# Kernel tuning notes

Measured on AMD Instinct MI355X. Metric: run time of the kernel, lower is better.

## Reference

```python
import jax, jax.numpy as jnp
import numpy as np

LSTM_SIZE = 32
NUM_OPS = 64
NUM_EDGE = 128
TEMPERATURE = 5.0
TANH_CONST = 2.5


def _lstm_cell(x, h, c, W_ih, W_hh, b_ih, b_hh):
    # PyTorch gate order: i, f, g, o
    g = x @ W_ih.T + b_ih + h @ W_hh.T + b_hh  # [4*H]
    i, f, gg, o = jnp.split(g, 4)
    c2 = jax.nn.sigmoid(f) * c + jax.nn.sigmoid(i) * jnp.tanh(gg)
    h2 = jax.nn.sigmoid(o) * jnp.tanh(c2)
    return h2, c2


def setup_inputs() -> dict:
    key = jax.random.key(0)
    ks = jax.random.split(key, 12)
    H, G, O = LSTM_SIZE, 4 * LSTM_SIZE, NUM_OPS
    s = 0.1
    return {
        "input_vars": jax.random.uniform(ks[0], (1, 1, H), jnp.float32, -s, s),
        "W_ih0": jax.random.uniform(ks[1], (G, H), jnp.float32, -s, s),
        "W_hh0": jax.random.uniform(ks[2], (G, H), jnp.float32, -s, s),
        "b_ih0": jax.random.uniform(ks[3], (G,), jnp.float32, -s, s),
        "b_hh0": jax.random.uniform(ks[4], (G,), jnp.float32, -s, s),
        "W_ih1": jax.random.uniform(ks[5], (G, H), jnp.float32, -s, s),
        "W_hh1": jax.random.uniform(ks[6], (G, H), jnp.float32, -s, s),
        "b_ih1": jax.random.uniform(ks[7], (G,), jnp.float32, -s, s),
        "b_hh1": jax.random.uniform(ks[8], (G,), jnp.float32, -s, s),
        "embd": jax.random.uniform(ks[9], (O, H), jnp.float32, -s, s),
        "W_pred": jax.random.uniform(ks[10], (O, H), jnp.float32, -s, s),
        "b_pred": jax.random.uniform(ks[11], (O,), jnp.float32, -s, s),
        "num_edge": NUM_EDGE,
    }


def reference(input_vars, W_ih0, W_hh0, b_ih0, b_hh0,
              W_ih1, W_hh1, b_ih1, b_hh1,
              embd, W_pred, b_pred, num_edge):
    H = input_vars.shape[-1]
    x0 = input_vars.reshape(H)
    z = jnp.zeros((H,), input_vars.dtype)
    key0 = jax.random.key(42)

    def step(carry, _):
        key, x, h0, c0, h1, c1 = carry
        h0, c0 = _lstm_cell(x, h0, c0, W_ih0, W_hh0, b_ih0, b_hh0)
        h1, c1 = _lstm_cell(h0, h1, c1, W_ih1, W_hh1, b_ih1, b_hh1)
        logits = TANH_CONST * jnp.tanh((h1 @ W_pred.T + b_pred) / TEMPERATURE)
        key, sub = jax.random.split(key)
        idx = jax.random.categorical(sub, logits)
        logp = jax.nn.log_softmax(logits)
        lp = logp[idx]
        ent = -jnp.sum(jnp.exp(logp) * logp)
        x = embd[idx]
        return (key, x, h0, c0, h1, c1), (lp, ent, idx)

    _, (lps, ents, arch) = jax.lax.scan(step, (key0, x0, z, z, z, z), None, length=num_edge)
    return jnp.sum(lps), jnp.sum(ents), arch
```

## Files before the change

kernel.cpp:

```cpp
#include <hip/hip_runtime.h>
#include <stdint.h>

namespace {

typedef float v2f __attribute__((ext_vector_type(2)));
typedef int   v2i __attribute__((ext_vector_type(2)));

constexpr int H      = 32;
constexpr int NEDGE  = 128;
constexpr float TINY   = 1.1754943508222875e-38f;
constexpr float L2E    = 1.4426950408889634f;
constexpr float LN2    = 0.6931471805599453f;

__device__ __forceinline__ void tf_round(uint32_t& x0, uint32_t& x1, int r) {
  x0 += x1;
  x1 = (x1 << r) | (x1 >> (32 - r));
  x1 ^= x0;
}

__device__ __forceinline__ void tf2x32(uint32_t k0, uint32_t k1,
                                       uint32_t& x0, uint32_t& x1) {
  const uint32_t ks2 = k0 ^ k1 ^ 0x1BD11BDAu;
  x0 += k0; x1 += k1;
  tf_round(x0,x1,13); tf_round(x0,x1,15); tf_round(x0,x1,26); tf_round(x0,x1, 6);
  x0 += k1;  x1 += ks2 + 1u;
  tf_round(x0,x1,17); tf_round(x0,x1,29); tf_round(x0,x1,16); tf_round(x0,x1,24);
  x0 += ks2; x1 += k0 + 2u;
  tf_round(x0,x1,13); tf_round(x0,x1,15); tf_round(x0,x1,26); tf_round(x0,x1, 6);
  x0 += k0;  x1 += k1 + 3u;
  tf_round(x0,x1,17); tf_round(x0,x1,29); tf_round(x0,x1,16); tf_round(x0,x1,24);
  x0 += k1;  x1 += ks2 + 4u;
  tf_round(x0,x1,13); tf_round(x0,x1,15); tf_round(x0,x1,26); tf_round(x0,x1, 6);
  x0 += ks2; x1 += k0 + 5u;
}

__device__ __forceinline__ float fexp(float x) {
  return __builtin_amdgcn_exp2f(x * L2E);
}
__device__ __forceinline__ float flog(float x) {
  return __builtin_amdgcn_logf(x) * LN2;
}
__device__ __forceinline__ float fsigmoid(float x) {
  return __builtin_amdgcn_rcpf(1.0f + __builtin_amdgcn_exp2f(-x * L2E));
}
__device__ __forceinline__ float ftanh(float x) {
  const float ax = __builtin_fabsf(x);
  const float t  = __builtin_amdgcn_exp2f(ax * (-2.0f * L2E));
  const float r  = (1.0f - t) * __builtin_amdgcn_rcpf(1.0f + t);
  return __builtin_copysignf(r, x);
}

__device__ __forceinline__ float rdlane(float v, int i) {
  return __int_as_float(__builtin_amdgcn_readlane(__float_as_int(v), i));
}

template <int CTRL>
__device__ __forceinline__ float dppf(float v) {
  return __int_as_float(__builtin_amdgcn_update_dpp(
      __float_as_int(v), __float_as_int(v), CTRL, 0xF, 0xF, false));
}

__device__ __forceinline__ float wave_sum64(float v) {
  v += dppf<0xB1>(v);
  v += dppf<0x4E>(v);
  v += dppf<0x141>(v);
  v += dppf<0x140>(v);
  return (rdlane(v, 15) + rdlane(v, 31)) + (rdlane(v, 47) + rdlane(v, 63));
}

__device__ __forceinline__ float wave_max64(float v) {
  v = fmaxf(v, dppf<0xB1>(v));
  v = fmaxf(v, dppf<0x4E>(v));
  v = fmaxf(v, dppf<0x141>(v));
  v = fmaxf(v, dppf<0x140>(v));
  return fmaxf(fmaxf(rdlane(v, 15), rdlane(v, 31)),
               fmaxf(rdlane(v, 47), rdlane(v, 63)));
}

__device__ __forceinline__ v2f pkfma(v2f a, v2f b, v2f c) {
  return __builtin_elementwise_fma(a, b, c);
}

__device__ __forceinline__ v2f permswap_pair(float g) {
  const v2i r = __builtin_amdgcn_permlane32_swap(
      __float_as_int(g), __float_as_int(g), false, false);
  return v2f{__int_as_float(r.x), __int_as_float(r.y)};
}

__global__ __launch_bounds__(192, 1)
void ctrl_kernel(const float* __restrict__ input_vars,
                 const float* __restrict__ W_ih0, const float* __restrict__ W_hh0,
                 const float* __restrict__ b_ih0, const float* __restrict__ b_hh0,
                 const float* __restrict__ W_ih1, const float* __restrict__ W_hh1,
                 const float* __restrict__ b_ih1, const float* __restrict__ b_hh1,
                 const float* __restrict__ embd,
                 const float* __restrict__ W_pred, const float* __restrict__ b_pred,
                 float* __restrict__ out) {
  const int tid  = threadIdx.x;
  const int lane = tid & 63;
  const int wid  = tid >> 6;
  const int rB   = lane + 64;

  __shared__ float4 Wh[2][8][128];
  __shared__ __align__(16) float embd_lds[65 * H];
  __shared__ __align__(16) float gumL[NEDGE][64];
  __shared__ __align__(16) float logitL[NEDGE][64];
  __shared__ __align__(16) float archL[NEDGE];
  __shared__ __align__(16) float h0bufD[2][H];
  __shared__ int h0flag;
  __shared__ int w1prog;
  __shared__ int gumflag;

  if (tid == 0) { h0flag = 0; w1prog = 0; gumflag = 0; }

  if (wid < 2) {
#define STAGE(MAT, SRC)                                                    \
  _Pragma("unroll")                                                        \
  for (int j = 0; j < 8; ++j) {                                            \
    const int i = (tid & 127) + 128 * j;                                   \
    const int k4 = i & 7, row = i >> 3;                                    \
    Wh[MAT][k4][row] = reinterpret_cast<const float4*>(SRC)[row * 8 + k4]; \
  }
    STAGE(0, W_hh0)
    STAGE(1, W_hh1)
#undef STAGE
  } else {
#pragma unroll
    for (int j = 0; j < 8; ++j)
      reinterpret_cast<float4*>(embd_lds)[lane + 64 * j] =
          reinterpret_cast<const float4*>(embd)[lane + 64 * j];
    if (lane < 8)
      reinterpret_cast<float4*>(&embd_lds[64 * H])[lane] =
          reinterpret_cast<const float4*>(input_vars)[lane];
  }
  __syncthreads();

  if (wid == 2) {
    uint32_t k0 = 0u, k1 = 42u;
    for (int t = 0; t < NEDGE; ++t) {
      uint32_t r0 = 0u, r1 = (uint32_t)(lane & 1);
      tf2x32(k0, k1, r0, r1);
      const uint32_t n0 = (uint32_t)__builtin_amdgcn_readlane((int)r0, 0);
      const uint32_t n1 = (uint32_t)__builtin_amdgcn_readlane((int)r1, 0);
      const uint32_t s0 = (uint32_t)__builtin_amdgcn_readlane((int)r0, 1);
      const uint32_t s1 = (uint32_t)__builtin_amdgcn_readlane((int)r1, 1);
      uint32_t x0 = 0u, x1 = (uint32_t)lane;
      tf2x32(s0, s1, x0, x1);
      const uint32_t bits = x0 ^ x1;
      k0 = n0; k1 = n1;
      float u = __uint_as_float(0x3f800000u | (bits >> 9)) - 1.0f;
      u = fmaxf(u + TINY, TINY);
      gumL[t][lane] = -flog(-flog(u));
      __threadfence_block();
      *(volatile int*)&gumflag = t + 1;
    }
    float lp_sum = 0.f, ent_sum = 0.f;
    for (int t = 0; t < NEDGE; ++t) {
      while (*(volatile int*)&w1prog < t + 1) { __builtin_amdgcn_s_sleep(1); }
      __threadfence_block();
      const float lg  = logitL[t][lane];
      const int  idxp = (int)archL[t];
      const float e  = fexp(lg);
      const float E  = wave_sum64(e);
      const float ES = wave_sum64(e * lg);
      const float lse = flog(E);
      const float li  = logitL[t][idxp];
      lp_sum  += li - lse;
      ent_sum += lse - ES / E;
    }
    if (lane == 0) { out[0] = lp_sum; out[1] = ent_sum; }
    return;
  }

  if (wid == 0) {
    float4 wxA0[8], wxB0[8];
#pragma unroll
    for (int q = 0; q < 8; ++q) {
      wxA0[q] = reinterpret_cast<const float4*>(W_ih0 + lane * H)[q];
      wxB0[q] = reinterpret_cast<const float4*>(W_ih0 + rB * H)[q];
    }
    const float bsum0A = b_ih0[lane] + b_hh0[lane];
    const float bsum0B = b_ih0[rB]   + b_hh0[rB];

    float c0 = 0.f, h0v = 0.f;
    v2f hoA01={0.f,0.f}, hoA23={0.f,0.f}, hoB01={0.f,0.f}, hoB23={0.f,0.f};
    float xdA, xdB;
    {
      v2f xA01={0.f,0.f}, xA23={0.f,0.f}, xB01={0.f,0.f}, xB23={0.f,0.f};
#pragma unroll
      for (int q = 0; q < 8; ++q) {
        const float4 x4 =
            *reinterpret_cast<const float4*>(&embd_lds[64 * H + 4 * q]);
        xA01 = pkfma(v2f{x4.x, x4.y}, v2f{wxA0[q].x, wxA0[q].y}, xA01);
        xA23 = pkfma(v2f{x4.z, x4.w}, v2f{wxA0[q].z, wxA0[q].w}, xA23);
        xB01 = pkfma(v2f{x4.x, x4.y}, v2f{wxB0[q].x, wxB0[q].y}, xB01);
        xB23 = pkfma(v2f{x4.z, x4.w}, v2f{wxB0[q].z, wxB0[q].w}, xB23);
      }
      xdA = (xA01.x + xA01.y) + (xA23.x + xA23.y);
      xdB = (xB01.x + xB01.y) + (xB23.x + xB23.y);
    }

    for (int t = 0; t < NEDGE; ++t) {
      const float gA = (bsum0A + xdA)
                     + ((hoA01.x + hoA01.y) + (hoA23.x + hoA23.y));
      const float gB = (bsum0B + xdB)
                     + ((hoB01.x + hoB01.y) + (hoB23.x + hoB23.y));
      const v2f gif = permswap_pair(gA);
      const v2f ggo = permswap_pair(gB);
      c0 = fsigmoid(gif.y) * c0 + fsigmoid(gif.x) * ftanh(ggo.x);
      h0v = fsigmoid(ggo.y) * ftanh(c0);
      h0bufD[t & 1][lane & 31] = h0v;
      __threadfence_block();
      *(volatile int*)&h0flag = t + 1;

      hoA01 = v2f{0.f,0.f}; hoA23 = v2f{0.f,0.f};
      hoB01 = v2f{0.f,0.f}; hoB23 = v2f{0.f,0.f};
#pragma unroll
      for (int q = 0; q < 8; ++q) {
        const float4 wA = Wh[0][q][lane];
        const float4 wB = Wh[0][q][rB];
        const v2f h01 = {rdlane(h0v, 4*q+0), rdlane(h0v, 4*q+1)};
        const v2f h23 = {rdlane(h0v, 4*q+2), rdlane(h0v, 4*q+3)};
        hoA01 = pkfma(h01, v2f{wA.x, wA.y}, hoA01);
        hoA23 = pkfma(h23, v2f{wA.z, wA.w}, hoA23);
        hoB01 = pkfma(h01, v2f{wB.x, wB.y}, hoB01);
        hoB23 = pkfma(h23, v2f{wB.z, wB.w}, hoB23);
      }

      if (t < NEDGE - 1) {
        while (*(volatile int*)&w1prog < t + 1) {}
        __threadfence_block();
        const int idxu = (int)archL[t];
        v2f xA01={0.f,0.f}, xA23={0.f,0.f}, xB01={0.f,0.f}, xB23={0.f,0.f};
#pragma unroll
        for (int q = 0; q < 8; ++q) {
          const float4 x4 =
              *reinterpret_cast<const float4*>(&embd_lds[idxu * H + 4 * q]);
          xA01 = pkfma(v2f{x4.x, x4.y}, v2f{wxA0[q].x, wxA0[q].y}, xA01);
          xA23 = pkfma(v2f{x4.z, x4.w}, v2f{wxA0[q].z, wxA0[q].w}, xA23);
          xB01 = pkfma(v2f{x4.x, x4.y}, v2f{wxB0[q].x, wxB0[q].y}, xB01);
          xB23 = pkfma(v2f{x4.z, x4.w}, v2f{wxB0[q].z, wxB0[q].w}, xB23);
        }
        xdA = (xA01.x + xA01.y) + (xA23.x + xA23.y);
        xdB = (xB01.x + xB01.y) + (xB23.x + xB23.y);
      }
    }
    return;
  }

  {
    float4 wx1A[8], wx1B[8], wp4[8];
#pragma unroll
    for (int q = 0; q < 8; ++q) {
      wx1A[q] = reinterpret_cast<const float4*>(W_ih1 + lane * H)[q];
      wx1B[q] = reinterpret_cast<const float4*>(W_ih1 + rB * H)[q];
      wp4[q]  = reinterpret_cast<const float4*>(W_pred + lane * H)[q];
    }
    const float bsum1A = b_ih1[lane] + b_hh1[lane];
    const float bsum1B = b_ih1[rB]   + b_hh1[rB];
    const float bp = b_pred[lane];

    float c1 = 0.f, h1v = 0.f;

    for (int t = 0; t < NEDGE; ++t) {
      v2f rA01={0.f,0.f}, rA23={0.f,0.f}, rB01={0.f,0.f}, rB23={0.f,0.f};
#pragma unroll
      for (int q = 0; q < 8; ++q) {
        const float4 wA = Wh[1][q][lane];
        const float4 wB = Wh[1][q][rB];
        const v2f h01 = {rdlane(h1v, 4*q+0), rdlane(h1v, 4*q+1)};
        const v2f h23 = {rdlane(h1v, 4*q+2), rdlane(h1v, 4*q+3)};
        rA01 = pkfma(h01, v2f{wA.x, wA.y}, rA01);
        rA23 = pkfma(h23, v2f{wA.z, wA.w}, rA23);
        rB01 = pkfma(h01, v2f{wB.x, wB.y}, rB01);
        rB23 = pkfma(h23, v2f{wB.z, wB.w}, rB23);
      }

      while (*(volatile int*)&gumflag < t + 1) {}
      __threadfence_block();
      const float gum = gumL[t][lane];

      while (*(volatile int*)&h0flag < t + 1) {}
      __threadfence_block();

#pragma unroll
      for (int q = 0; q < 8; ++q) {
        const float4 h4 =
            *reinterpret_cast<const float4*>(&h0bufD[t & 1][4 * q]);
        rA01 = pkfma(v2f{h4.x, h4.y}, v2f{wx1A[q].x, wx1A[q].y}, rA01);
        rA23 = pkfma(v2f{h4.z, h4.w}, v2f{wx1A[q].z, wx1A[q].w}, rA23);
        rB01 = pkfma(v2f{h4.x, h4.y}, v2f{wx1B[q].x, wx1B[q].y}, rB01);
        rB23 = pkfma(v2f{h4.z, h4.w}, v2f{wx1B[q].z, wx1B[q].w}, rB23);
      }
      const float gA1 = bsum1A + ((rA01.x + rA01.y) + (rA23.x + rA23.y));
      const float gB1 = bsum1B + ((rB01.x + rB01.y) + (rB23.x + rB23.y));
      const v2f gif1 = permswap_pair(gA1);
      const v2f ggo1 = permswap_pair(gB1);
      c1  = fsigmoid(gif1.y) * c1 + fsigmoid(gif1.x) * ftanh(ggo1.x);
      h1v = fsigmoid(ggo1.y) * ftanh(c1);

      v2f p01 = {0.f, 0.f}, p23 = {0.f, 0.f};
#pragma unroll
      for (int q = 0; q < 8; ++q) {
        const float4 w = wp4[q];
        p01 = pkfma(v2f{rdlane(h1v, 4*q+0), rdlane(h1v, 4*q+1)},
                    v2f{w.x, w.y}, p01);
        p23 = pkfma(v2f{rdlane(h1v, 4*q+2), rdlane(h1v, 4*q+3)},
                    v2f{w.z, w.w}, p23);
      }
      const float pre   = bp + ((p01.x + p01.y) + (p23.x + p23.y));
      const float logit = 2.5f * ftanh(pre * 0.2f);
      const float pert  = logit + gum;

      const float M = wave_max64(pert);
      const unsigned long long msk = __ballot(pert == M);
      const int idxu = __ffsll((long long)msk) - 1;

      archL[t] = (float)idxu;
      logitL[t][lane] = logit;
      __threadfence_block();
      *(volatile int*)&w1prog = t + 1;
    }

    out[2 + lane]      = archL[lane];
    out[2 + 64 + lane] = archL[64 + lane];
  }
}

}

extern "C" void kernel_launch(void* const* d_in, const int* in_sizes, int n_in,
                              void* d_out, int out_size, void* d_ws, size_t ws_size,
                              hipStream_t stream) {
  (void)in_sizes; (void)n_in; (void)d_ws; (void)ws_size; (void)out_size;
  const float* input_vars = (const float*)d_in[0];
  const float* W_ih0 = (const float*)d_in[1];
  const float* W_hh0 = (const float*)d_in[2];
  const float* b_ih0 = (const float*)d_in[3];
  const float* b_hh0 = (const float*)d_in[4];
  const float* W_ih1 = (const float*)d_in[5];
  const float* W_hh1 = (const float*)d_in[6];
  const float* b_ih1 = (const float*)d_in[7];
  const float* b_hh1 = (const float*)d_in[8];
  const float* embd  = (const float*)d_in[9];
  const float* W_pred = (const float*)d_in[10];
  const float* b_pred = (const float*)d_in[11];
  float* out = (float*)d_out;

  hipLaunchKernelGGL(ctrl_kernel, dim3(1), dim3(192), 0, stream,
                     input_vars, W_ih0, W_hh0, b_ih0, b_hh0,
                     W_ih1, W_hh1, b_ih1, b_hh1,
                     embd, W_pred, b_pred, out);
}
```

Measured before the change: 148.4 us.

## Restructure wave roles: precompute embedding projections, offload recurrent matvecs to helper wave

```diff
diff --git a/kernel.cpp b/kernel.cpp
--- a/kernel.cpp
+++ b/kernel.cpp
@@ -101,37 +101,27 @@
   const int wid  = tid >> 6;
   const int rB   = lane + 64;
 
-  __shared__ float4 Wh[2][8][128];
   __shared__ __align__(16) float embd_lds[65 * H];
+  __shared__ __align__(16) float xdot[65][128];
+  __shared__ __align__(16) float h0buf[2][H];
+  __shared__ __align__(16) float h1buf[2][H];
+  __shared__ __align__(16) float4 hob0[2][2][64];
+  __shared__ __align__(16) float4 hob1[2][2][64];
   __shared__ __align__(16) float gumL[NEDGE][64];
   __shared__ __align__(16) float logitL[NEDGE][64];
   __shared__ __align__(16) float archL[NEDGE];
-  __shared__ __align__(16) float h0bufD[2][H];
-  __shared__ int h0flag;
-  __shared__ int w1prog;
-  __shared__ int gumflag;
-
-  if (tid == 0) { h0flag = 0; w1prog = 0; gumflag = 0; }
+  __shared__ int h0f, h1f, ho0f, ho1f, gumf, smf;
+
+  if (tid == 0) { h0f = 0; h1f = 0; ho0f = 0; ho1f = 0; gumf = 0; smf = 0; }
 
   if (wid < 2) {
-#define STAGE(MAT, SRC)                                                    \
-  _Pragma("unroll")                                                        \
-  for (int j = 0; j < 8; ++j) {                                            \
-    const int i = (tid & 127) + 128 * j;                                   \
-    const int k4 = i & 7, row = i >> 3;                                    \
-    Wh[MAT][k4][row] = reinterpret_cast<const float4*>(SRC)[row * 8 + k4]; \
-  }
-    STAGE(0, W_hh0)
-    STAGE(1, W_hh1)
-#undef STAGE
-  } else {
-#pragma unroll
-    for (int j = 0; j < 8; ++j)
-      reinterpret_cast<float4*>(embd_lds)[lane + 64 * j] =
-          reinterpret_cast<const float4*>(embd)[lane + 64 * j];
-    if (lane < 8)
-      reinterpret_cast<float4*>(&embd_lds[64 * H])[lane] =
-          reinterpret_cast<const float4*>(input_vars)[lane];
+#pragma unroll
+    for (int j = 0; j < 4; ++j)
+      reinterpret_cast<float4*>(embd_lds)[(tid & 127) + 128 * j] =
+          reinterpret_cast<const float4*>(embd)[(tid & 127) + 128 * j];
+    if (tid < 8)
+      reinterpret_cast<float4*>(&embd_lds[64 * H])[tid] =
+          reinterpret_cast<const float4*>(input_vars)[tid];
   }
   __syncthreads();
 
@@ -152,11 +142,11 @@
       u = fmaxf(u + TINY, TINY);
       gumL[t][lane] = -flog(-flog(u));
       __threadfence_block();
-      *(volatile int*)&gumflag = t + 1;
+      *(volatile int*)&gumf = t + 1;
     }
     float lp_sum = 0.f, ent_sum = 0.f;
     for (int t = 0; t < NEDGE; ++t) {
-      while (*(volatile int*)&w1prog < t + 1) { __builtin_amdgcn_s_sleep(1); }
+      while (*(volatile int*)&smf < t + 1) { __builtin_amdgcn_s_sleep(1); }
       __threadfence_block();
       const float lg  = logitL[t][lane];
       const int  idxp = (int)archL[t];
@@ -172,159 +162,184 @@
     return;
   }
 
-  if (wid == 0) {
+  if (wid == 1) {
+    float4 whA0[8], whB0[8], whA1[8], whB1[8];
+#pragma unroll
+    for (int q = 0; q < 8; ++q) {
+      whA0[q] = reinterpret_cast<const float4*>(W_hh0 + lane * H)[q];
+      whB0[q] = reinterpret_cast<const float4*>(W_hh0 + rB * H)[q];
+      whA1[q] = reinterpret_cast<const float4*>(W_hh1 + lane * H)[q];
+      whB1[q] = reinterpret_cast<const float4*>(W_hh1 + rB * H)[q];
+    }
+    for (int t = 0; t < NEDGE; ++t) {
+      while (*(volatile int*)&h0f < t + 1) { __builtin_amdgcn_s_sleep(1); }
+      __threadfence_block();
+      {
+        v2f a01={0.f,0.f}, a23={0.f,0.f}, b01={0.f,0.f}, b23={0.f,0.f};
+#pragma unroll
+        for (int q = 0; q < 8; ++q) {
+          const float4 h4 =
+              *reinterpret_cast<const float4*>(&h0buf[t & 1][4 * q]);
+          const v2f h01 = {h4.x, h4.y};
+          const v2f h23 = {h4.z, h4.w};
+          a01 = pkfma(h01, v2f{whA0[q].x, whA0[q].y}, a01);
+          a23 = pkfma(h23, v2f{whA0[q].z, whA0[q].w}, a23);
+          b01 = pkfma(h01, v2f{whB0[q].x, whB0[q].y}, b01);
+          b23 = pkfma(h23, v2f{whB0[q].z, whB0[q].w}, b23);
+        }
+        hob0[t & 1][0][lane] = make_float4(a01.x, a01.y, a23.x, a23.y);
+        hob0[t & 1][1][lane] = make_float4(b01.x, b01.y, b23.x, b23.y);
+        __threadfence_block();
+        *(volatile int*)&ho0f = t + 1;
+      }
+      while (*(volatile int*)&h1f < t + 1) { __builtin_amdgcn_s_sleep(1); }
+      __threadfence_block();
+      {
+        v2f a01={0.f,0.f}, a23={0.f,0.f}, b01={0.f,0.f}, b23={0.f,0.f};
+#pragma unroll
+        for (int q = 0; q < 8; ++q) {
+          const float4 h4 =
+              *reinterpret_cast<const float4*>(&h1buf[t & 1][4 * q]);
+          const v2f h01 = {h4.x, h4.y};
+          const v2f h23 = {h4.z, h4.w};
+          a01 = pkfma(h01, v2f{whA1[q].x, whA1[q].y}, a01);
+          a23 = pkfma(h23, v2f{whA1[q].z, whA1[q].w}, a23);
+          b01 = pkfma(h01, v2f{whB1[q].x, whB1[q].y}, b01);
+          b23 = pkfma(h23, v2f{whB1[q].z, whB1[q].w}, b23);
+        }
+        hob1[t & 1][0][lane] = make_float4(a01.x, a01.y, a23.x, a23.y);
+        hob1[t & 1][1][lane] = make_float4(b01.x, b01.y, b23.x, b23.y);
+        __threadfence_block();
+        *(volatile int*)&ho1f = t + 1;
+      }
+    }
+    return;
+  }
+
+  {
     float4 wxA0[8], wxB0[8];
 #pragma unroll
     for (int q = 0; q < 8; ++q) {
       wxA0[q] = reinterpret_cast<const float4*>(W_ih0 + lane * H)[q];
       wxB0[q] = reinterpret_cast<const float4*>(W_ih0 + rB * H)[q];
     }
-    const float bsum0A = b_ih0[lane] + b_hh0[lane];
-    const float bsum0B = b_ih0[rB]   + b_hh0[rB];
-
-    float c0 = 0.f, h0v = 0.f;
-    v2f hoA01={0.f,0.f}, hoA23={0.f,0.f}, hoB01={0.f,0.f}, hoB23={0.f,0.f};
-    float xdA, xdB;
-    {
+    for (int op = 0; op < 65; ++op) {
       v2f xA01={0.f,0.f}, xA23={0.f,0.f}, xB01={0.f,0.f}, xB23={0.f,0.f};
 #pragma unroll
       for (int q = 0; q < 8; ++q) {
         const float4 x4 =
-            *reinterpret_cast<const float4*>(&embd_lds[64 * H + 4 * q]);
+            *reinterpret_cast<const float4*>(&embd_lds[op * H + 4 * q]);
         xA01 = pkfma(v2f{x4.x, x4.y}, v2f{wxA0[q].x, wxA0[q].y}, xA01);
         xA23 = pkfma(v2f{x4.z, x4.w}, v2f{wxA0[q].z, wxA0[q].w}, xA23);
         xB01 = pkfma(v2f{x4.x, x4.y}, v2f{wxB0[q].x, wxB0[q].y}, xB01);
         xB23 = pkfma(v2f{x4.z, x4.w}, v2f{wxB0[q].z, wxB0[q].w}, xB23);
       }
-      xdA = (xA01.x + xA01.y) + (xA23.x + xA23.y);
-      xdB = (xB01.x + xB01.y) + (xB23.x + xB23.y);
-    }
-
-    for (int t = 0; t < NEDGE; ++t) {
-      const float gA = (bsum0A + xdA)
-                     + ((hoA01.x + hoA01.y) + (hoA23.x + hoA23.y));
-      const float gB = (bsum0B + xdB)
-                     + ((hoB01.x + hoB01.y) + (hoB23.x + hoB23.y));
+      xdot[op][lane] = (xA01.x + xA01.y) + (xA23.x + xA23.y);
+      xdot[op][rB]   = (xB01.x + xB01.y) + (xB23.x + xB23.y);
+    }
+  }
+  float4 wx1A[8], wx1B[8], wp4[8];
+#pragma unroll
+  for (int q = 0; q < 8; ++q) {
+    wx1A[q] = reinterpret_cast<const float4*>(W_ih1 + lane * H)[q];
+    wx1B[q] = reinterpret_cast<const float4*>(W_ih1 + rB * H)[q];
+    wp4[q]  = reinterpret_cast<const float4*>(W_pred + lane * H)[q];
+  }
+  const float bsum0A = b_ih0[lane] + b_hh0[lane];
+  const float bsum0B = b_ih0[rB]   + b_hh0[rB];
+  const float bsum1A = b_ih1[lane] + b_hh1[lane];
+  const float bsum1B = b_ih1[rB]   + b_hh1[rB];
+  const float bp = b_pred[lane];
+
+  float c0 = 0.f, h0v = 0.f, c1 = 0.f, h1v = 0.f;
+  float xdA = xdot[64][lane], xdB = xdot[64][rB];
+
+  for (int t = 0; t < NEDGE; ++t) {
+    float hoSumA, hoSumB;
+    if (t > 0) {
+      while (*(volatile int*)&ho0f < t) {}
+      __threadfence_block();
+      const float4 a = hob0[(t - 1) & 1][0][lane];
+      const float4 b = hob0[(t - 1) & 1][1][lane];
+      hoSumA = (a.x + a.y) + (a.z + a.w);
+      hoSumB = (b.x + b.y) + (b.z + b.w);
+    } else { hoSumA = 0.f; hoSumB = 0.f; }
+    {
+      const float gA = (bsum0A + xdA) + hoSumA;
+      const float gB = (bsum0B + xdB) + hoSumB;
       const v2f gif = permswap_pair(gA);
       const v2f ggo = permswap_pair(gB);
       c0 = fsigmoid(gif.y) * c0 + fsigmoid(gif.x) * ftanh(ggo.x);
       h0v = fsigmoid(ggo.y) * ftanh(c0);
-      h0bufD[t & 1][lane & 31] = h0v;
-      __threadfence_block();
-      *(volatile int*)&h0flag = t + 1;
-
-      hoA01 = v2f{0.f,0.f}; hoA23 = v2f{0.f,0.f};
-      hoB01 = v2f{0.f,0.f}; hoB23 = v2f{0.f,0.f};
-#pragma unroll
-      for (int q = 0; q < 8; ++q) {
-        const float4 wA = Wh[0][q][lane];
-        const float4 wB = Wh[0][q][rB];
-        const v2f h01 = {rdlane(h0v, 4*q+0), rdlane(h0v, 4*q+1)};
-        const v2f h23 = {rdlane(h0v, 4*q+2), rdlane(h0v, 4*q+3)};
-        hoA01 = pkfma(h01, v2f{wA.x, wA.y}, hoA01);
-        hoA23 = pkfma(h23, v2f{wA.z, wA.w}, hoA23);
-        hoB01 = pkfma(h01, v2f{wB.x, wB.y}, hoB01);
-        hoB23 = pkfma(h23, v2f{wB.z, wB.w}, hoB23);
-      }
-
-      if (t < NEDGE - 1) {
-        while (*(volatile int*)&w1prog < t + 1) {}
-        __threadfence_block();
-        const int idxu = (int)archL[t];
-        v2f xA01={0.f,0.f}, xA23={0.f,0.f}, xB01={0.f,0.f}, xB23={0.f,0.f};
-#pragma unroll
-        for (int q = 0; q < 8; ++q) {
-          const float4 x4 =
-              *reinterpret_cast<const float4*>(&embd_lds[idxu * H + 4 * q]);
-          xA01 = pkfma(v2f{x4.x, x4.y}, v2f{wxA0[q].x, wxA0[q].y}, xA01);
-          xA23 = pkfma(v2f{x4.z, x4.w}, v2f{wxA0[q].z, wxA0[q].w}, xA23);
-          xB01 = pkfma(v2f{x4.x, x4.y}, v2f{wxB0[q].x, wxB0[q].y}, xB01);
-          xB23 = pkfma(v2f{x4.z, x4.w}, v2f{wxB0[q].z, wxB0[q].w}, xB23);
-        }
-        xdA = (xA01.x + xA01.y) + (xA23.x + xA23.y);
-        xdB = (xB01.x + xB01.y) + (xB23.x + xB23.y);
-      }
-    }
-    return;
-  }
-
-  {
-    float4 wx1A[8], wx1B[8], wp4[8];
+      h0buf[t & 1][lane & 31] = h0v;
+      __threadfence_block();
+      *(volatile int*)&h0f = t + 1;
+    }
+
+    v2f rA01, rA23, rB01, rB23;
+    if (t > 0) {
+      while (*(volatile int*)&ho1f < t) {}
+      __threadfence_block();
+      const float4 a = hob1[(t - 1) & 1][0][lane];
+      const float4 b = hob1[(t - 1) & 1][1][lane];
+      rA01 = v2f{a.x, a.y}; rA23 = v2f{a.z, a.w};
+      rB01 = v2f{b.x, b.y}; rB23 = v2f{b.z, b.w};
+    } else {
+      rA01 = v2f{0.f,0.f}; rA23 = v2f{0.f,0.f};
+      rB01 = v2f{0.f,0.f}; rB23 = v2f{0.f,0.f};
+    }
 #pragma unroll
     for (int q = 0; q < 8; ++q) {
-      wx1A[q] = reinterpret_cast<const float4*>(W_ih1 + lane * H)[q];
-      wx1B[q] = reinterpret_cast<const float4*>(W_ih1 + rB * H)[q];
-      wp4[q]  = reinterpret_cast<const float4*>(W_pred + lane * H)[q];
-    }
-    const float bsum1A = b_ih1[lane] + b_hh1[lane];
-    const float bsum1B = b_ih1[rB]   + b_hh1[rB];
-    const float bp = b_pred[lane];
-
-    float c1 = 0.f, h1v = 0.f;
-
-    for (int t = 0; t < NEDGE; ++t) {
-      v2f rA01={0.f,0.f}, rA23={0.f,0.f}, rB01={0.f,0.f}, rB23={0.f,0.f};
-#pragma unroll
-      for (int q = 0; q < 8; ++q) {
-        const float4 wA = Wh[1][q][lane];
-        const float4 wB = Wh[1][q][rB];
-        const v2f h01 = {rdlane(h1v, 4*q+0), rdlane(h1v, 4*q+1)};
-        const v2f h23 = {rdlane(h1v, 4*q+2), rdlane(h1v, 4*q+3)};
-        rA01 = pkfma(h01, v2f{wA.x, wA.y}, rA01);
-        rA23 = pkfma(h23, v2f{wA.z, wA.w}, rA23);
-        rB01 = pkfma(h01, v2f{wB.x, wB.y}, rB01);
-        rB23 = pkfma(h23, v2f{wB.z, wB.w}, rB23);
-      }
-
-      while (*(volatile int*)&gumflag < t + 1) {}
-      __threadfence_block();
-      const float gum = gumL[t][lane];
-
-      while (*(volatile int*)&h0flag < t + 1) {}
-      __threadfence_block();
-
-#pragma unroll
-      for (int q = 0; q < 8; ++q) {
-        const float4 h4 =
-            *reinterpret_cast<const float4*>(&h0bufD[t & 1][4 * q]);
-        rA01 = pkfma(v2f{h4.x, h4.y}, v2f{wx1A[q].x, wx1A[q].y}, rA01);
-        rA23 = pkfma(v2f{h4.z, h4.w}, v2f{wx1A[q].z, wx1A[q].w}, rA23);
-        rB01 = pkfma(v2f{h4.x, h4.y}, v2f{wx1B[q].x, wx1B[q].y}, rB01);
-        rB23 = pkfma(v2f{h4.z, h4.w}, v2f{wx1B[q].z, wx1B[q].w}, rB23);
-      }
+      const v2f h01 = {rdlane(h0v, 4*q+0), rdlane(h0v, 4*q+1)};
+      const v2f h23 = {rdlane(h0v, 4*q+2), rdlane(h0v, 4*q+3)};
+      rA01 = pkfma(h01, v2f{wx1A[q].x, wx1A[q].y}, rA01);
+      rA23 = pkfma(h23, v2f{wx1A[q].z, wx1A[q].w}, rA23);
+      rB01 = pkfma(h01, v2f{wx1B[q].x, wx1B[q].y}, rB01);
+      rB23 = pkfma(h23, v2f{wx1B[q].z, wx1B[q].w}, rB23);
+    }
+    {
       const float gA1 = bsum1A + ((rA01.x + rA01.y) + (rA23.x + rA23.y));
       const float gB1 = bsum1B + ((rB01.x + rB01.y) + (rB23.x + rB23.y));
       const v2f gif1 = permswap_pair(gA1);
       const v2f ggo1 = permswap_pair(gB1);
       c1  = fsigmoid(gif1.y) * c1 + fsigmoid(gif1.x) * ftanh(ggo1.x);
       h1v = fsigmoid(ggo1.y) * ftanh(c1);
-
-      v2f p01 = {0.f, 0.f}, p23 = {0.f, 0.f};
-#pragma unroll
-      for (int q = 0; q < 8; ++q) {
-        const float4 w = wp4[q];
-        p01 = pkfma(v2f{rdlane(h1v, 4*q+0), rdlane(h1v, 4*q+1)},
-                    v2f{w.x, w.y}, p01);
-        p23 = pkfma(v2f{rdlane(h1v, 4*q+2), rdlane(h1v, 4*q+3)},
-                    v2f{w.z, w.w}, p23);
-      }
-      const float pre   = bp + ((p01.x + p01.y) + (p23.x + p23.y));
-      const float logit = 2.5f * ftanh(pre * 0.2f);
-      const float pert  = logit + gum;
-
-      const float M = wave_max64(pert);
-      const unsigned long long msk = __ballot(pert == M);
-      const int idxu = __ffsll((long long)msk) - 1;
-
-      archL[t] = (float)idxu;
-      logitL[t][lane] = logit;
-      __threadfence_block();
-      *(volatile int*)&w1prog = t + 1;
-    }
-
-    out[2 + lane]      = archL[lane];
-    out[2 + 64 + lane] = archL[64 + lane];
-  }
+      h1buf[t & 1][lane & 31] = h1v;
+      __threadfence_block();
+      *(volatile int*)&h1f = t + 1;
+    }
+
+    v2f p01 = {0.f, 0.f}, p23 = {0.f, 0.f};
+#pragma unroll
+    for (int q = 0; q < 8; ++q) {
+      const float4 w = wp4[q];
+      p01 = pkfma(v2f{rdlane(h1v, 4*q+0), rdlane(h1v, 4*q+1)},
+                  v2f{w.x, w.y}, p01);
+      p23 = pkfma(v2f{rdlane(h1v, 4*q+2), rdlane(h1v, 4*q+3)},
+                  v2f{w.z, w.w}, p23);
+    }
+    const float pre   = bp + ((p01.x + p01.y) + (p23.x + p23.y));
+    const float logit = 2.5f * ftanh(pre * 0.2f);
+
+    while (*(volatile int*)&gumf < t + 1) {}
+    __threadfence_block();
+    const float pert = logit + gumL[t][lane];
+
+    const float M = wave_max64(pert);
+    const unsigned long long msk = __ballot(pert == M);
+    const int idxu = __ffsll((long long)msk) - 1;
+
+    archL[t] = (float)idxu;
+    logitL[t][lane] = logit;
+    __threadfence_block();
+    *(volatile int*)&smf = t + 1;
+
+    xdA = xdot[idxu][lane];
+    xdB = xdot[idxu][rB];
+  }
+
+  out[2 + lane]      = archL[lane];
+  out[2 + 64 + lane] = archL[64 + lane];
 }
 
 }
```

Result: faster. 140.2 us (-5.5%).
